# Kernel tuning notes

Measured on AMD Instinct MI355X. Metric: run time of the kernel, lower is better.

Reference implementation:

```python
import jax, jax.numpy as jnp
import numpy as np

B, T, F, H = 8, 1024, 1024, 16
DK = F // H


def setup_inputs() -> dict:
    key = jax.random.key(0)
    ks = jax.random.split(key, 12)
    s = 1.0 / np.sqrt(F)
    return {
        "query": jax.random.normal(ks[0], (B, T, F), jnp.float32),
        "key": jax.random.normal(ks[1], (B, T, F), jnp.float32),
        "value": jax.random.normal(ks[2], (B, T, F), jnp.float32),
        "mask": jnp.ones((B, T), jnp.float32),
        "Wq": jax.random.normal(ks[3], (F, F), jnp.float32) * s,
        "bq": jax.random.normal(ks[4], (F,), jnp.float32) * s,
        "Wk": jax.random.normal(ks[5], (F, F), jnp.float32) * s,
        "bk": jax.random.normal(ks[6], (F,), jnp.float32) * s,
        "Wv": jax.random.normal(ks[7], (F, F), jnp.float32) * s,
        "bv": jax.random.normal(ks[8], (F,), jnp.float32) * s,
        "Wo": jax.random.normal(ks[9], (F, F), jnp.float32) * s,
        "bo": jax.random.normal(ks[10], (F,), jnp.float32) * s,
    }


def reference(query, key, value, mask, Wq, bq, Wk, bk, Wv, bv, Wo, bo):
    # projections, split into heads: (B, H, T, DK)
    def proj(x, W, b):
        y = x @ W.T + b
        return y.reshape(B, -1, H, DK).transpose(0, 2, 1, 3)

    q = proj(query, Wq, bq)
    k = proj(key, Wk, bk)
    v = proj(value, Wv, bv)

    scores = jnp.einsum("bhqd,bhkd->bhqk", q, k) / jnp.sqrt(jnp.float32(DK))
    attn = jax.nn.softmax(scores, axis=-1)  # dropout is identity (eval / p=0)
    x = jnp.einsum("bhqk,bhkd->bhqd", attn, v)
    x = x.transpose(0, 2, 1, 3).reshape(B, -1, F)
    x = x @ Wo.T + bo
    return x * mask[..., None]
```

## Files before the change

### kernel.cpp

```cpp
#include <hip/hip_runtime.h>
#include <hip/hip_bf16.h>

typedef unsigned short u16;
typedef unsigned int u32;
typedef __attribute__((ext_vector_type(8))) short bf16x8;
typedef __attribute__((ext_vector_type(8))) unsigned short u16x8;
typedef __attribute__((ext_vector_type(4))) unsigned short u16x4;
typedef __attribute__((ext_vector_type(4))) float f32x4;

#define DEVI __device__ __forceinline__

static constexpr int Bn = 8, Tn = 1024, Fn = 1024, Hn = 16, DKn = 64;
static constexpr int Mtot = Bn * Tn;

DEVI u16 f2bf(float x) {
  unsigned u = __builtin_bit_cast(unsigned, x);
  u += 0x7fffu + ((u >> 16) & 1u);
  return (u16)(u >> 16);
}

DEVI u32 cvt_pk_bf16(float lo, float hi) {
  u32 r;
  asm("v_cvt_pk_bf16_f32 %0, %1, %2" : "=v"(r) : "v"(lo), "v"(hi));
  return r;
}

DEVI f32x4 mfma16(bf16x8 a, bf16x8 b, f32x4 c) {
  return __builtin_amdgcn_mfma_f32_16x16x32_bf16(a, b, c, 0, 0, 0);
}

typedef const __attribute__((address_space(1))) void GAS;
typedef __attribute__((address_space(3))) void LAS;
#define GLL16(gp, lp) __builtin_amdgcn_global_load_lds((GAS*)(gp), (LAS*)(lp), 16, 0, 0)

DEVI void cvt_chunk(const float* __restrict__ in, u16* __restrict__ out, int i) {
  const float4* p = reinterpret_cast<const float4*>(in + i);
  float4 a = p[0], b = p[1];
  float v[8] = {a.x, a.y, a.z, a.w, b.x, b.y, b.z, b.w};
  u16x8 r;
#pragma unroll
  for (int j = 0; j < 8; j++) r[j] = f2bf(v[j]);
  *reinterpret_cast<u16x8*>(out + i) = r;
}

__global__ __launch_bounds__(256) void cvt3(const float* __restrict__ a, const float* __restrict__ b,
                                            const float* __restrict__ c, u16* __restrict__ oa,
                                            u16* __restrict__ ob, u16* __restrict__ oc) {
  const int id = blockIdx.x * 256 + threadIdx.x;
  const int seg = id >> 20;
  const int off = (id & 1048575) * 8;
  const float* s = seg == 0 ? a : (seg == 1 ? b : c);
  u16* d = seg == 0 ? oa : (seg == 1 ? ob : oc);
  cvt_chunk(s, d, off);
}

__global__ __launch_bounds__(256) void cvt4(const float* __restrict__ a, const float* __restrict__ b,
                                            const float* __restrict__ c, const float* __restrict__ e,
                                            u16* __restrict__ oa, u16* __restrict__ ob,
                                            u16* __restrict__ oc, u16* __restrict__ oe) {
  const int id = blockIdx.x * 256 + threadIdx.x;
  const int seg = id >> 17;
  const int off = (id & 131071) * 8;
  const float* s = seg == 0 ? a : (seg == 1 ? b : (seg == 2 ? c : e));
  u16* d = seg == 0 ? oa : (seg == 1 ? ob : (seg == 2 ? oc : oe));
  cvt_chunk(s, d, off);
}

template <int MODE>
__global__ __launch_bounds__(512, 1) void gemm8(const u16* __restrict__ A,
                                                const u16* __restrict__ Bw,
                                                const float* __restrict__ bias,
                                                const float* __restrict__ mask,
                                                u16* __restrict__ Obf,
                                                float* __restrict__ Of,
                                                float oscale) {
  constexpr int Kd = 1024;
  __shared__ u16 sA[2][256 * 64];
  __shared__ u16 sB[2][128 * 64];
  const int tid = threadIdx.x;
  const int l = tid & 63, w = tid >> 6;
  const int wm = w >> 1, wn = w & 1;
  const int lr = l & 15, g = l >> 4;
  const int bid = blockIdx.x;
  const int wg = (bid & 7) * 32 + (bid >> 3);
  const int m0 = (wg >> 3) * 256, n0 = (wg & 7) * 128;

  f32x4 acc[4][4];
#pragma unroll
  for (int i = 0; i < 4; i++)
#pragma unroll
    for (int j = 0; j < 4; j++) acc[i][j] = f32x4{0.f, 0.f, 0.f, 0.f};

  int aoff[4], boff[2];
#pragma unroll
  for (int i = 0; i < 4; i++) {
    const int c = i * 512 + tid;
    const int r = c >> 3, cc = (c & 7) ^ (r & 7);
    aoff[i] = r * Kd + cc * 8;
  }
#pragma unroll
  for (int i = 0; i < 2; i++) {
    const int c = i * 512 + tid;
    const int r = c >> 3, cc = (c & 7) ^ (r & 7);
    boff[i] = r * Kd + cc * 8;
  }
  const u16* Abase = A + (size_t)m0 * Kd;
  const u16* Bbase = Bw + (size_t)n0 * Kd;

  auto stage = [&](int buf, int kt) {
#pragma unroll
    for (int i = 0; i < 4; i++)
      GLL16(Abase + kt * 64 + aoff[i], (char*)&sA[buf][0] + (i * 512 + w * 64) * 16);
#pragma unroll
    for (int i = 0; i < 2; i++)
      GLL16(Bbase + kt * 64 + boff[i], (char*)&sB[buf][0] + (i * 512 + w * 64) * 16);
  };

  stage(0, 0);
  for (int t = 0; t < 16; ++t) {
    const int cur = t & 1;
    if (t < 15) {
      stage(cur ^ 1, t + 1);
      asm volatile("s_waitcnt vmcnt(6)" ::: "memory");
    } else {
      asm volatile("s_waitcnt vmcnt(0)" ::: "memory");
    }
    asm volatile("s_barrier" ::: "memory");
#pragma unroll
    for (int ks = 0; ks < 2; ks++) {
      bf16x8 af[4], bfr[4];
#pragma unroll
      for (int mi = 0; mi < 4; mi++) {
        const int row = wm * 64 + mi * 16 + lr;
        af[mi] = *reinterpret_cast<const bf16x8*>(
            (const char*)&sA[cur][0] + row * 128 + ((ks * 64 + g * 16) ^ ((row & 7) << 4)));
      }
#pragma unroll
      for (int ni = 0; ni < 4; ni++) {
        const int row = wn * 64 + ni * 16 + lr;
        bfr[ni] = *reinterpret_cast<const bf16x8*>(
            (const char*)&sB[cur][0] + row * 128 + ((ks * 64 + g * 16) ^ ((row & 7) << 4)));
      }
      __builtin_amdgcn_s_setprio(1);
#pragma unroll
      for (int mi = 0; mi < 4; mi++)
#pragma unroll
        for (int ni = 0; ni < 4; ni++) {
          if constexpr (MODE == 1)
            acc[mi][ni] = mfma16(af[mi], bfr[ni], acc[mi][ni]);
          else
            acc[ni][mi] = mfma16(bfr[ni], af[mi], acc[ni][mi]);
        }
      __builtin_amdgcn_s_setprio(0);
    }
    asm volatile("s_barrier" ::: "memory");
  }

  if constexpr (MODE == 1) {
#pragma unroll
    for (int ni = 0; ni < 4; ni++) {
      const int n = n0 + wn * 64 + ni * 16 + lr;
      const float bv = bias[n];
      const int h = n >> 6, dk = n & 63;
#pragma unroll
      for (int mi = 0; mi < 4; mi++) {
        const int mb = m0 + wm * 64 + mi * 16 + g * 4;
        u16x4 pk;
#pragma unroll
        for (int j = 0; j < 4; j++) pk[j] = f2bf(acc[mi][ni][j] + bv);
        const int b = mb >> 10, tt = mb & 1023;
        size_t idx = (((size_t)b * 16 + h) * 64 + dk) * 1024 + tt;
        *reinterpret_cast<u16x4*>(Obf + idx) = pk;
      }
    }
  } else {
#pragma unroll
    for (int ni = 0; ni < 4; ni++) {
      const int nb = n0 + wn * 64 + ni * 16 + g * 4;
      const float4 b4 = *reinterpret_cast<const float4*>(&bias[nb]);
#pragma unroll
      for (int mi = 0; mi < 4; mi++) {
        const int m = m0 + wm * 64 + mi * 16 + lr;
        const f32x4 a = acc[ni][mi];
        if constexpr (MODE == 0) {
          const int b = m >> 10, tt = m & 1023;
          const int h = nb >> 6, dk0 = nb & 63;
          u16x4 pk;
          pk[0] = f2bf((a[0] + b4.x) * oscale);
          pk[1] = f2bf((a[1] + b4.y) * oscale);
          pk[2] = f2bf((a[2] + b4.z) * oscale);
          pk[3] = f2bf((a[3] + b4.w) * oscale);
          *reinterpret_cast<u16x4*>(&Obf[((((size_t)b * 16 + h) * 1024 + tt) * 64) + dk0]) = pk;
        } else {
          const float mk = mask[m];
          float4 o;
          o.x = (a[0] + b4.x) * mk;
          o.y = (a[1] + b4.y) * mk;
          o.z = (a[2] + b4.z) * mk;
          o.w = (a[3] + b4.w) * mk;
          *reinterpret_cast<float4*>(&Of[(size_t)m * 1024 + nb]) = o;
        }
      }
    }
  }
}

__global__ __launch_bounds__(256, 4) void flash_attn(const u16* __restrict__ Qb,
                                                     const u16* __restrict__ Kb,
                                                     const u16* __restrict__ Vt,
                                                     u16* __restrict__ ctx) {
  __shared__ u16 sK[2][64 * 64];
  __shared__ u16 sV[64 * 64];
  __shared__ u16 pbuf[4][16 * 64];
  const int tid = threadIdx.x, l = tid & 63, w = tid >> 6;
  const int lr = l & 15, g = l >> 4;
  const int wg = ((blockIdx.x & 7) << 7) + (blockIdx.x >> 3);
  const int qt = wg & 7, bh = wg >> 3;
  const u16* Qh = Qb + (size_t)bh * (Tn * DKn);
  const u16* Kh = Kb + (size_t)bh * (Tn * DKn);
  const u16* Vh = Vt + (size_t)bh * (Tn * DKn);

  bf16x8 aq[2][2];
  int qrow[2];
#pragma unroll
  for (int qg = 0; qg < 2; qg++) {
    qrow[qg] = qt * 128 + w * 32 + qg * 16 + lr;
    aq[qg][0] = *reinterpret_cast<const bf16x8*>(Qh + (size_t)qrow[qg] * 64 + g * 8);
    aq[qg][1] = *reinterpret_cast<const bf16x8*>(Qh + (size_t)qrow[qg] * 64 + 32 + g * 8);
  }

  float mrow[2] = {-1e30f, -1e30f}, lsum[2] = {0.f, 0.f};
  f32x4 of[2][4];
#pragma unroll
  for (int qg = 0; qg < 2; qg++)
#pragma unroll
    for (int c = 0; c < 4; c++) of[qg][c] = f32x4{0.f, 0.f, 0.f, 0.f};

  char* pb = (char*)&pbuf[w][0];
  const int sw = (lr & 7) << 4;
  int wadr[4];
#pragma unroll
  for (int c = 0; c < 4; c++) wadr[c] = lr * 128 + (((c * 16 + g * 4) * 2) ^ sw);
  const int radr0 = lr * 128 + ((g * 16) ^ sw);
  const int radr1 = lr * 128 + ((64 + g * 16) ^ sw);

  auto stageK = [&](int buf, int kv0) {
#pragma unroll
    for (int i = 0; i < 2; i++) {
      const int tt = i * 256 + tid;
      const int r = tt >> 3;
      const int c = (tt & 7) ^ (r & 7);
      GLL16((const char*)Kh + ((size_t)(kv0 + r) << 7) + (c << 4),
            (char*)&sK[buf][0] + i * 4096 + w * 1024);
    }
  };
  auto stageV = [&](int kv0) {
#pragma unroll
    for (int i = 0; i < 2; i++) {
      const int tt = i * 256 + tid;
      const int r = tt >> 3;
      const int c = (tt & 7) ^ (r & 7);
      GLL16((const char*)Vh + ((size_t)r << 11) + kv0 * 2 + (c << 4),
            (char*)&sV[0] + i * 4096 + w * 1024);
    }
  };

  stageK(0, 0);
  stageV(0);
  __syncthreads();
  int cur = 0;

  for (int t = 0; t < 16; t++) {
    if (t < 15) stageK(cur ^ 1, (t + 1) * 64);
    const char* kb = (const char*)&sK[cur][0];
    const char* vb = (const char*)&sV[0];

    f32x4 sf[2][4];
    __builtin_amdgcn_s_setprio(1);
#pragma unroll
    for (int c = 0; c < 4; c++) {
      const char* kr = kb + (c * 16 + lr) * 128;
      bf16x8 k0 = *reinterpret_cast<const bf16x8*>(kr + ((g * 16) ^ sw));
      bf16x8 k1 = *reinterpret_cast<const bf16x8*>(kr + ((64 + g * 16) ^ sw));
      f32x4 z0 = mfma16(k0, aq[0][0], f32x4{0.f, 0.f, 0.f, 0.f});
      sf[0][c] = mfma16(k1, aq[0][1], z0);
      f32x4 z1 = mfma16(k0, aq[1][0], f32x4{0.f, 0.f, 0.f, 0.f});
      sf[1][c] = mfma16(k1, aq[1][1], z1);
    }
    __builtin_amdgcn_s_setprio(0);

    bf16x8 ap[2][2];
#pragma unroll
    for (int qg = 0; qg < 2; qg++) {
      f32x4 mx4 = sf[qg][0];
#pragma unroll
      for (int c = 1; c < 4; c++)
#pragma unroll
        for (int j = 0; j < 4; j++) mx4[j] = fmaxf(mx4[j], sf[qg][c][j]);
      const float pmax = fmaxf(fmaxf(mx4[0], mx4[1]), fmaxf(mx4[2], mx4[3]));
      if (__any(pmax > mrow[qg] + 8.0f)) {
        float mx = pmax;
        mx = fmaxf(mx, __shfl_xor(mx, 16));
        mx = fmaxf(mx, __shfl_xor(mx, 32));
        const float mn = fmaxf(mrow[qg], mx);
        const float alpha = exp2f(mrow[qg] - mn);
        mrow[qg] = mn;
        lsum[qg] *= alpha;
#pragma unroll
        for (int c = 0; c < 4; c++)
#pragma unroll
          for (int j = 0; j < 4; j++) of[qg][c][j] *= alpha;
      }
      const float mn = mrow[qg];
      float rs = 0.f;
#pragma unroll
      for (int c = 0; c < 4; c++)
#pragma unroll
        for (int j = 0; j < 4; j++) {
          float p = exp2f(sf[qg][c][j] - mn);
          sf[qg][c][j] = p;
          rs += p;
        }
      lsum[qg] += rs;

#pragma unroll
      for (int c = 0; c < 4; c++) {
        uint2 pk;
        pk.x = cvt_pk_bf16(sf[qg][c][0], sf[qg][c][1]);
        pk.y = cvt_pk_bf16(sf[qg][c][2], sf[qg][c][3]);
        *reinterpret_cast<uint2*>(pb + wadr[c]) = pk;
      }
      ap[qg][0] = *reinterpret_cast<const bf16x8*>(pb + radr0);
      ap[qg][1] = *reinterpret_cast<const bf16x8*>(pb + radr1);
    }

    __syncthreads();

    __builtin_amdgcn_s_setprio(1);
#pragma unroll
    for (int d0 = 0; d0 < 4; d0++) {
      const char* vr = vb + (d0 * 16 + lr) * 128;
      bf16x8 v0 = *reinterpret_cast<const bf16x8*>(vr + ((g * 16) ^ sw));
      bf16x8 v1 = *reinterpret_cast<const bf16x8*>(vr + ((64 + g * 16) ^ sw));
#pragma unroll
      for (int qg = 0; qg < 2; qg++) {
        f32x4 z = mfma16(v0, ap[qg][0], of[qg][d0]);
        of[qg][d0] = mfma16(v1, ap[qg][1], z);
      }
    }
    __builtin_amdgcn_s_setprio(0);

    __syncthreads();
    if (t < 15) stageV((t + 1) * 64);
    cur ^= 1;
  }

  const int b = bh >> 4, h = bh & 15;
#pragma unroll
  for (int qg = 0; qg < 2; qg++) {
    float ls = lsum[qg];
    ls += __shfl_xor(ls, 16);
    ls += __shfl_xor(ls, 32);
    const float inv = 1.0f / ls;
    const size_t base = ((size_t)b * 1024 + qrow[qg]) * 1024 + h * 64;
#pragma unroll
    for (int d0 = 0; d0 < 4; d0++) {
      uint2 pk;
      pk.x = cvt_pk_bf16(of[qg][d0][0] * inv, of[qg][d0][1] * inv);
      pk.y = cvt_pk_bf16(of[qg][d0][2] * inv, of[qg][d0][3] * inv);
      *reinterpret_cast<uint2*>(ctx + base + d0 * 16 + g * 4) = pk;
    }
  }
}

extern "C" void kernel_launch(void* const* d_in, const int* in_sizes, int n_in,
                              void* d_out, int out_size, void* d_ws, size_t ws_size,
                              hipStream_t stream) {
  const float* query = (const float*)d_in[0];
  const float* key = (const float*)d_in[1];
  const float* value = (const float*)d_in[2];
  const float* mask = (const float*)d_in[3];
  const float* Wq = (const float*)d_in[4];
  const float* bq = (const float*)d_in[5];
  const float* Wk = (const float*)d_in[6];
  const float* bk = (const float*)d_in[7];
  const float* Wv = (const float*)d_in[8];
  const float* bv = (const float*)d_in[9];
  const float* Wo = (const float*)d_in[10];
  const float* bo = (const float*)d_in[11];
  (void)in_sizes; (void)n_in; (void)out_size; (void)ws_size;

  u16* ws = (u16*)d_ws;
  const size_t MB8 = (size_t)8 << 20;
  u16* Xq = ws;
  u16* Xk = ws + MB8;
  u16* Xv = ws + 2 * MB8;
  u16* Wqb = ws + 3 * MB8;
  u16* Wkb = Wqb + (1 << 20);
  u16* Wvb = Wkb + (1 << 20);
  u16* Wob = Wvb + (1 << 20);
  u16* Qb = Wob + (1 << 20);
  u16* Kb = Qb + MB8;
  u16* Vtb = Kb + MB8;
  u16* ctx = Xq;

  cvt3<<<12288, 256, 0, stream>>>(query, key, value, Xq, Xk, Xv);
  cvt4<<<2048, 256, 0, stream>>>(Wq, Wk, Wv, Wo, Wqb, Wkb, Wvb, Wob);

  const float SC = 0.125f * 1.44269504089f;
  const int ng = (Mtot / 256) * (Fn / 128);
  gemm8<0><<<ng, 512, 0, stream>>>(Xq, Wqb, bq, nullptr, Qb, nullptr, SC);
  gemm8<0><<<ng, 512, 0, stream>>>(Xk, Wkb, bk, nullptr, Kb, nullptr, 1.0f);
  gemm8<1><<<ng, 512, 0, stream>>>(Xv, Wvb, bv, nullptr, Vtb, nullptr, 1.0f);

  flash_attn<<<Bn * Hn * (Tn / 128), 256, 0, stream>>>(Qb, Kb, Vtb, ctx);

  gemm8<2><<<ng, 512, 0, stream>>>(ctx, Wob, bo, mask, nullptr, (float*)d_out, 1.0f);
}
```

Before: 198.1 us.

## Halve flash-attention query tile to 64 rows per block

Each attention workgroup now covers 64 query rows, one 16-row MFMA group per wave, instead of 128 rows with two groups per wave. The grid doubles to 2048 blocks and launch bounds rise to 5 blocks per CU, with the block-to-(batch, head, tile) mapping updated to match. The aim is to cut register pressure and raise occupancy and latency hiding. In exchange, every K/V tile staged in LDS is reused by half as many queries, doubling K/V staging traffic per unit of work. The output-projection GEMM launch count is written as a literal equal to the previous computed value.

```diff
diff --git a/kernel.cpp b/kernel.cpp
--- a/kernel.cpp
+++ b/kernel.cpp
@@ -205,7 +205,7 @@
   }
 }
 
-__global__ __launch_bounds__(256, 4) void flash_attn(const u16* __restrict__ Qb,
+__global__ __launch_bounds__(256, 5) void flash_attn(const u16* __restrict__ Qb,
                                                      const u16* __restrict__ Kb,
                                                      const u16* __restrict__ Vt,
                                                      u16* __restrict__ ctx) {
@@ -214,27 +214,20 @@
   __shared__ u16 pbuf[4][16 * 64];
   const int tid = threadIdx.x, l = tid & 63, w = tid >> 6;
   const int lr = l & 15, g = l >> 4;
-  const int wg = ((blockIdx.x & 7) << 7) + (blockIdx.x >> 3);
-  const int qt = wg & 7, bh = wg >> 3;
+  const int wg = ((blockIdx.x & 7) << 8) + (blockIdx.x >> 3);
+  const int qt = wg & 15, bh = wg >> 4;
   const u16* Qh = Qb + (size_t)bh * (Tn * DKn);
   const u16* Kh = Kb + (size_t)bh * (Tn * DKn);
   const u16* Vh = Vt + (size_t)bh * (Tn * DKn);
 
-  bf16x8 aq[2][2];
-  int qrow[2];
-#pragma unroll
-  for (int qg = 0; qg < 2; qg++) {
-    qrow[qg] = qt * 128 + w * 32 + qg * 16 + lr;
-    aq[qg][0] = *reinterpret_cast<const bf16x8*>(Qh + (size_t)qrow[qg] * 64 + g * 8);
-    aq[qg][1] = *reinterpret_cast<const bf16x8*>(Qh + (size_t)qrow[qg] * 64 + 32 + g * 8);
-  }
-
-  float mrow[2] = {-1e30f, -1e30f}, lsum[2] = {0.f, 0.f};
-  f32x4 of[2][4];
-#pragma unroll
-  for (int qg = 0; qg < 2; qg++)
-#pragma unroll
-    for (int c = 0; c < 4; c++) of[qg][c] = f32x4{0.f, 0.f, 0.f, 0.f};
+  const int qrow = qt * 64 + w * 16 + lr;
+  const bf16x8 aq0 = *reinterpret_cast<const bf16x8*>(Qh + (size_t)qrow * 64 + g * 8);
+  const bf16x8 aq1 = *reinterpret_cast<const bf16x8*>(Qh + (size_t)qrow * 64 + 32 + g * 8);
+
+  float mrow = -1e30f, lsum = 0.f;
+  f32x4 of[4];
+#pragma unroll
+  for (int c = 0; c < 4; c++) of[c] = f32x4{0.f, 0.f, 0.f, 0.f};
 
   char* pb = (char*)&pbuf[w][0];
   const int sw = (lr & 7) << 4;
@@ -275,64 +268,57 @@
     const char* kb = (const char*)&sK[cur][0];
     const char* vb = (const char*)&sV[0];
 
-    f32x4 sf[2][4];
+    f32x4 sf[4];
     __builtin_amdgcn_s_setprio(1);
 #pragma unroll
     for (int c = 0; c < 4; c++) {
       const char* kr = kb + (c * 16 + lr) * 128;
       bf16x8 k0 = *reinterpret_cast<const bf16x8*>(kr + ((g * 16) ^ sw));
       bf16x8 k1 = *reinterpret_cast<const bf16x8*>(kr + ((64 + g * 16) ^ sw));
-      f32x4 z0 = mfma16(k0, aq[0][0], f32x4{0.f, 0.f, 0.f, 0.f});
-      sf[0][c] = mfma16(k1, aq[0][1], z0);
-      f32x4 z1 = mfma16(k0, aq[1][0], f32x4{0.f, 0.f, 0.f, 0.f});
-      sf[1][c] = mfma16(k1, aq[1][1], z1);
+      f32x4 z = mfma16(k0, aq0, f32x4{0.f, 0.f, 0.f, 0.f});
+      sf[c] = mfma16(k1, aq1, z);
     }
     __builtin_amdgcn_s_setprio(0);
 
-    bf16x8 ap[2][2];
-#pragma unroll
-    for (int qg = 0; qg < 2; qg++) {
-      f32x4 mx4 = sf[qg][0];
-#pragma unroll
-      for (int c = 1; c < 4; c++)
-#pragma unroll
-        for (int j = 0; j < 4; j++) mx4[j] = fmaxf(mx4[j], sf[qg][c][j]);
-      const float pmax = fmaxf(fmaxf(mx4[0], mx4[1]), fmaxf(mx4[2], mx4[3]));
-      if (__any(pmax > mrow[qg] + 8.0f)) {
-        float mx = pmax;
-        mx = fmaxf(mx, __shfl_xor(mx, 16));
-        mx = fmaxf(mx, __shfl_xor(mx, 32));
-        const float mn = fmaxf(mrow[qg], mx);
-        const float alpha = exp2f(mrow[qg] - mn);
-        mrow[qg] = mn;
-        lsum[qg] *= alpha;
-#pragma unroll
-        for (int c = 0; c < 4; c++)
-#pragma unroll
-          for (int j = 0; j < 4; j++) of[qg][c][j] *= alpha;
-      }
-      const float mn = mrow[qg];
-      float rs = 0.f;
+    f32x4 mx4 = sf[0];
+#pragma unroll
+    for (int c = 1; c < 4; c++)
+#pragma unroll
+      for (int j = 0; j < 4; j++) mx4[j] = fmaxf(mx4[j], sf[c][j]);
+    const float pmax = fmaxf(fmaxf(mx4[0], mx4[1]), fmaxf(mx4[2], mx4[3]));
+    if (__any(pmax > mrow + 8.0f)) {
+      float mx = pmax;
+      mx = fmaxf(mx, __shfl_xor(mx, 16));
+      mx = fmaxf(mx, __shfl_xor(mx, 32));
+      const float mn = fmaxf(mrow, mx);
+      const float alpha = exp2f(mrow - mn);
+      mrow = mn;
+      lsum *= alpha;
 #pragma unroll
       for (int c = 0; c < 4; c++)
 #pragma unroll
-        for (int j = 0; j < 4; j++) {
-          float p = exp2f(sf[qg][c][j] - mn);
-          sf[qg][c][j] = p;
-          rs += p;
-        }
-      lsum[qg] += rs;
-
-#pragma unroll
-      for (int c = 0; c < 4; c++) {
-        uint2 pk;
-        pk.x = cvt_pk_bf16(sf[qg][c][0], sf[qg][c][1]);
-        pk.y = cvt_pk_bf16(sf[qg][c][2], sf[qg][c][3]);
-        *reinterpret_cast<uint2*>(pb + wadr[c]) = pk;
-      }
-      ap[qg][0] = *reinterpret_cast<const bf16x8*>(pb + radr0);
-      ap[qg][1] = *reinterpret_cast<const bf16x8*>(pb + radr1);
-    }
+        for (int j = 0; j < 4; j++) of[c][j] *= alpha;
+    }
+    float rs = 0.f;
+#pragma unroll
+    for (int c = 0; c < 4; c++)
+#pragma unroll
+      for (int j = 0; j < 4; j++) {
+        float pp = exp2f(sf[c][j] - mrow);
+        sf[c][j] = pp;
+        rs += pp;
+      }
+    lsum += rs;
+
+#pragma unroll
+    for (int c = 0; c < 4; c++) {
+      uint2 pk;
+      pk.x = cvt_pk_bf16(sf[c][0], sf[c][1]);
+      pk.y = cvt_pk_bf16(sf[c][2], sf[c][3]);
+      *reinterpret_cast<uint2*>(pb + wadr[c]) = pk;
+    }
+    const bf16x8 ap0 = *reinterpret_cast<const bf16x8*>(pb + radr0);
+    const bf16x8 ap1 = *reinterpret_cast<const bf16x8*>(pb + radr1);
 
     __syncthreads();
 
@@ -342,11 +328,8 @@
       const char* vr = vb + (d0 * 16 + lr) * 128;
       bf16x8 v0 = *reinterpret_cast<const bf16x8*>(vr + ((g * 16) ^ sw));
       bf16x8 v1 = *reinterpret_cast<const bf16x8*>(vr + ((64 + g * 16) ^ sw));
-#pragma unroll
-      for (int qg = 0; qg < 2; qg++) {
-        f32x4 z = mfma16(v0, ap[qg][0], of[qg][d0]);
-        of[qg][d0] = mfma16(v1, ap[qg][1], z);
-      }
+      f32x4 z = mfma16(v0, ap0, of[d0]);
+      of[d0] = mfma16(v1, ap1, z);
     }
     __builtin_amdgcn_s_setprio(0);
 
@@ -355,21 +338,18 @@
     cur ^= 1;
   }
 
+  float ls = lsum;
+  ls += __shfl_xor(ls, 16);
+  ls += __shfl_xor(ls, 32);
+  const float inv = 1.0f / ls;
   const int b = bh >> 4, h = bh & 15;
-#pragma unroll
-  for (int qg = 0; qg < 2; qg++) {
-    float ls = lsum[qg];
-    ls += __shfl_xor(ls, 16);
-    ls += __shfl_xor(ls, 32);
-    const float inv = 1.0f / ls;
-    const size_t base = ((size_t)b * 1024 + qrow[qg]) * 1024 + h * 64;
-#pragma unroll
-    for (int d0 = 0; d0 < 4; d0++) {
-      uint2 pk;
-      pk.x = cvt_pk_bf16(of[qg][d0][0] * inv, of[qg][d0][1] * inv);
-      pk.y = cvt_pk_bf16(of[qg][d0][2] * inv, of[qg][d0][3] * inv);
-      *reinterpret_cast<uint2*>(ctx + base + d0 * 16 + g * 4) = pk;
-    }
+  const size_t base = ((size_t)b * 1024 + qrow) * 1024 + h * 64;
+#pragma unroll
+  for (int d0 = 0; d0 < 4; d0++) {
+    uint2 pk;
+    pk.x = cvt_pk_bf16(of[d0][0] * inv, of[d0][1] * inv);
+    pk.y = cvt_pk_bf16(of[d0][2] * inv, of[d0][3] * inv);
+    *reinterpret_cast<uint2*>(ctx + base + d0 * 16 + g * 4) = pk;
   }
 }
 
@@ -413,7 +393,7 @@
   gemm8<0><<<ng, 512, 0, stream>>>(Xk, Wkb, bk, nullptr, Kb, nullptr, 1.0f);
   gemm8<1><<<ng, 512, 0, stream>>>(Xv, Wvb, bv, nullptr, Vtb, nullptr, 1.0f);
 
-  flash_attn<<<Bn * Hn * (Tn / 128), 256, 0, stream>>>(Qb, Kb, Vtb, ctx);
-
-  gemm8<2><<<ng, 512, 0, stream>>>(ctx, Wob, bo, mask, nullptr, (float*)d_out, 1.0f);
-}
+  flash_attn<<<Bn * Hn * (Tn / 64), 256, 0, stream>>>(Qb, Kb, Vtb, ctx);
+
+  gemm8<2><<<256, 512, 0, stream>>>(ctx, Wob, bo, mask, nullptr, (float*)d_out, 1.0f);
+}
```

Result: slower. 204.1 us (+3.1%).

## Merge Q/K/V projection GEMMs into one launch and split A/B staging

Applied to the files above, without the earlier changes.

The three separate projection GEMM launches become a single launch with a 3-wide grid dimension that selects inputs, weights, bias and output layout per block. This removes two kernel launches and the tail idle time at the end of each one. The GEMM core now prefetches the A tile before the barrier but issues the B tile prefetch after the first k-substep's MFMAs, which spreads global loads across compute. In exchange, the runtime branch on the projection index adds code size and register pressure, and the different wait count changes how much load latency the pipeline hides.

```diff
diff --git a/kernel.cpp b/kernel.cpp
--- a/kernel.cpp
+++ b/kernel.cpp
@@ -66,15 +66,171 @@
   cvt_chunk(s, d, off);
 }
 
-template <int MODE>
-__global__ __launch_bounds__(512, 1) void gemm8(const u16* __restrict__ A,
-                                                const u16* __restrict__ Bw,
-                                                const float* __restrict__ bias,
-                                                const float* __restrict__ mask,
-                                                u16* __restrict__ Obf,
-                                                float* __restrict__ Of,
-                                                float oscale) {
+template <int SWAP>
+DEVI void gemm_core_run(const u16* __restrict__ A, const u16* __restrict__ Bw,
+                        int m0, int n0, int tid, u16* sA0, u16* sA1, u16* sB0, u16* sB1,
+                        f32x4 (&acc)[4][4]) {
   constexpr int Kd = 1024;
+  const int l = tid & 63, w = tid >> 6;
+  const int wm = w >> 1, wn = w & 1;
+  const int lr = l & 15, g = l >> 4;
+
+  int aoff[4], boff[2];
+#pragma unroll
+  for (int i = 0; i < 4; i++) {
+    const int c = i * 512 + tid;
+    const int r = c >> 3, cc = (c & 7) ^ (r & 7);
+    aoff[i] = r * Kd + cc * 8;
+  }
+#pragma unroll
+  for (int i = 0; i < 2; i++) {
+    const int c = i * 512 + tid;
+    const int r = c >> 3, cc = (c & 7) ^ (r & 7);
+    boff[i] = r * Kd + cc * 8;
+  }
+  const u16* Ab = A + (size_t)m0 * Kd;
+  const u16* Bb = Bw + (size_t)n0 * Kd;
+  u16* sAp[2] = {sA0, sA1};
+  u16* sBp[2] = {sB0, sB1};
+
+  auto stageA = [&](int buf, int kt) {
+#pragma unroll
+    for (int i = 0; i < 4; i++)
+      GLL16(Ab + kt * 64 + aoff[i], (char*)sAp[buf] + (i * 512 + w * 64) * 16);
+  };
+  auto stageB = [&](int buf, int kt) {
+#pragma unroll
+    for (int i = 0; i < 2; i++)
+      GLL16(Bb + kt * 64 + boff[i], (char*)sBp[buf] + (i * 512 + w * 64) * 16);
+  };
+
+  stageA(0, 0);
+  stageB(0, 0);
+  for (int t = 0; t < 16; ++t) {
+    const int cur = t & 1;
+    const char* cA = (const char*)sAp[cur];
+    const char* cB = (const char*)sBp[cur];
+    if (t < 15) {
+      stageA(cur ^ 1, t + 1);
+      asm volatile("s_waitcnt vmcnt(4)" ::: "memory");
+    } else {
+      asm volatile("s_waitcnt vmcnt(0)" ::: "memory");
+    }
+    asm volatile("s_barrier" ::: "memory");
+#pragma unroll
+    for (int ks = 0; ks < 2; ks++) {
+      bf16x8 af[4], bfr[4];
+#pragma unroll
+      for (int mi = 0; mi < 4; mi++) {
+        const int row = wm * 64 + mi * 16 + lr;
+        af[mi] = *reinterpret_cast<const bf16x8*>(cA + row * 128 +
+                                                  ((ks * 64 + g * 16) ^ ((row & 7) << 4)));
+      }
+#pragma unroll
+      for (int ni = 0; ni < 4; ni++) {
+        const int row = wn * 64 + ni * 16 + lr;
+        bfr[ni] = *reinterpret_cast<const bf16x8*>(cB + row * 128 +
+                                                   ((ks * 64 + g * 16) ^ ((row & 7) << 4)));
+      }
+      __builtin_amdgcn_s_setprio(1);
+#pragma unroll
+      for (int mi = 0; mi < 4; mi++)
+#pragma unroll
+        for (int ni = 0; ni < 4; ni++) {
+          if constexpr (SWAP)
+            acc[ni][mi] = mfma16(bfr[ni], af[mi], acc[ni][mi]);
+          else
+            acc[mi][ni] = mfma16(af[mi], bfr[ni], acc[mi][ni]);
+        }
+      __builtin_amdgcn_s_setprio(0);
+      if (ks == 0 && t < 15) stageB(cur ^ 1, t + 1);
+    }
+    asm volatile("s_barrier" ::: "memory");
+  }
+}
+
+DEVI void gemm_core_run_rt(const u16* __restrict__ A, const u16* __restrict__ Bw,
+                           int m0, int n0, int tid, bool swap, u16* sA0, u16* sA1,
+                           u16* sB0, u16* sB1, f32x4 (&acc)[4][4]) {
+  if (swap)
+    gemm_core_run<1>(A, Bw, m0, n0, tid, sA0, sA1, sB0, sB1, acc);
+  else
+    gemm_core_run<0>(A, Bw, m0, n0, tid, sA0, sA1, sB0, sB1, acc);
+}
+
+__global__ __launch_bounds__(512, 1) void qkv_gemm(
+    const u16* __restrict__ Xq, const u16* __restrict__ Xk, const u16* __restrict__ Xv,
+    const u16* __restrict__ Wq, const u16* __restrict__ Wk, const u16* __restrict__ Wv,
+    const float* __restrict__ bq, const float* __restrict__ bk, const float* __restrict__ bv,
+    u16* __restrict__ Qo, u16* __restrict__ Ko, u16* __restrict__ Vo, float SC) {
+  __shared__ u16 sA[2][256 * 64];
+  __shared__ u16 sB[2][128 * 64];
+  const int tid = threadIdx.x;
+  const int l = tid & 63, w = tid >> 6;
+  const int wm = w >> 1, wn = w & 1;
+  const int lr = l & 15, g = l >> 4;
+  const int p = blockIdx.y;
+  const u16* A = p == 0 ? Xq : (p == 1 ? Xk : Xv);
+  const u16* Bw = p == 0 ? Wq : (p == 1 ? Wk : Wv);
+  const float* bias = p == 0 ? bq : (p == 1 ? bk : bv);
+  u16* Obf = p == 0 ? Qo : (p == 1 ? Ko : Vo);
+  const float oscale = p == 0 ? SC : 1.0f;
+  const int bid = blockIdx.x;
+  const int wg = (bid & 7) * 32 + (bid >> 3);
+  const int m0 = (wg >> 3) * 256, n0 = (wg & 7) * 128;
+
+  f32x4 acc[4][4];
+#pragma unroll
+  for (int i = 0; i < 4; i++)
+#pragma unroll
+    for (int j = 0; j < 4; j++) acc[i][j] = f32x4{0.f, 0.f, 0.f, 0.f};
+
+  gemm_core_run_rt(A, Bw, m0, n0, tid, p != 2, sA[0], sA[1], sB[0], sB[1], acc);
+
+  if (p == 2) {
+#pragma unroll
+    for (int ni = 0; ni < 4; ni++) {
+      const int n = n0 + wn * 64 + ni * 16 + lr;
+      const float bvv = bias[n];
+      const int h = n >> 6, dk = n & 63;
+#pragma unroll
+      for (int mi = 0; mi < 4; mi++) {
+        const int mb = m0 + wm * 64 + mi * 16 + g * 4;
+        u16x4 pk;
+#pragma unroll
+        for (int j = 0; j < 4; j++) pk[j] = f2bf(acc[mi][ni][j] + bvv);
+        const int b = mb >> 10, tt = mb & 1023;
+        size_t idx = (((size_t)b * 16 + h) * 64 + dk) * 1024 + tt;
+        *reinterpret_cast<u16x4*>(Obf + idx) = pk;
+      }
+    }
+  } else {
+#pragma unroll
+    for (int ni = 0; ni < 4; ni++) {
+      const int nb = n0 + wn * 64 + ni * 16 + g * 4;
+      const float4 b4 = *reinterpret_cast<const float4*>(&bias[nb]);
+#pragma unroll
+      for (int mi = 0; mi < 4; mi++) {
+        const int m = m0 + wm * 64 + mi * 16 + lr;
+        const f32x4 a = acc[ni][mi];
+        const int b = m >> 10, tt = m & 1023;
+        const int h = nb >> 6, dk0 = nb & 63;
+        u16x4 pk;
+        pk[0] = f2bf((a[0] + b4.x) * oscale);
+        pk[1] = f2bf((a[1] + b4.y) * oscale);
+        pk[2] = f2bf((a[2] + b4.z) * oscale);
+        pk[3] = f2bf((a[3] + b4.w) * oscale);
+        *reinterpret_cast<u16x4*>(&Obf[((((size_t)b * 16 + h) * 1024 + tt) * 64) + dk0]) = pk;
+      }
+    }
+  }
+}
+
+__global__ __launch_bounds__(512, 1) void gemm_out(const u16* __restrict__ A,
+                                                   const u16* __restrict__ Bw,
+                                                   const float* __restrict__ bias,
+                                                   const float* __restrict__ mask,
+                                                   float* __restrict__ Of) {
   __shared__ u16 sA[2][256 * 64];
   __shared__ u16 sB[2][128 * 64];
   const int tid = threadIdx.x;
@@ -91,116 +247,23 @@
 #pragma unroll
     for (int j = 0; j < 4; j++) acc[i][j] = f32x4{0.f, 0.f, 0.f, 0.f};
 
-  int aoff[4], boff[2];
-#pragma unroll
-  for (int i = 0; i < 4; i++) {
-    const int c = i * 512 + tid;
-    const int r = c >> 3, cc = (c & 7) ^ (r & 7);
-    aoff[i] = r * Kd + cc * 8;
-  }
-#pragma unroll
-  for (int i = 0; i < 2; i++) {
-    const int c = i * 512 + tid;
-    const int r = c >> 3, cc = (c & 7) ^ (r & 7);
-    boff[i] = r * Kd + cc * 8;
-  }
-  const u16* Abase = A + (size_t)m0 * Kd;
-  const u16* Bbase = Bw + (size_t)n0 * Kd;
-
-  auto stage = [&](int buf, int kt) {
-#pragma unroll
-    for (int i = 0; i < 4; i++)
-      GLL16(Abase + kt * 64 + aoff[i], (char*)&sA[buf][0] + (i * 512 + w * 64) * 16);
-#pragma unroll
-    for (int i = 0; i < 2; i++)
-      GLL16(Bbase + kt * 64 + boff[i], (char*)&sB[buf][0] + (i * 512 + w * 64) * 16);
-  };
-
-  stage(0, 0);
-  for (int t = 0; t < 16; ++t) {
-    const int cur = t & 1;
-    if (t < 15) {
-      stage(cur ^ 1, t + 1);
-      asm volatile("s_waitcnt vmcnt(6)" ::: "memory");
-    } else {
-      asm volatile("s_waitcnt vmcnt(0)" ::: "memory");
-    }
-    asm volatile("s_barrier" ::: "memory");
-#pragma unroll
-    for (int ks = 0; ks < 2; ks++) {
-      bf16x8 af[4], bfr[4];
-#pragma unroll
-      for (int mi = 0; mi < 4; mi++) {
-        const int row = wm * 64 + mi * 16 + lr;
-        af[mi] = *reinterpret_cast<const bf16x8*>(
-            (const char*)&sA[cur][0] + row * 128 + ((ks * 64 + g * 16) ^ ((row & 7) << 4)));
-      }
-#pragma unroll
-      for (int ni = 0; ni < 4; ni++) {
-        const int row = wn * 64 + ni * 16 + lr;
-        bfr[ni] = *reinterpret_cast<const bf16x8*>(
-            (const char*)&sB[cur][0] + row * 128 + ((ks * 64 + g * 16) ^ ((row & 7) << 4)));
-      }
-      __builtin_amdgcn_s_setprio(1);
-#pragma unroll
-      for (int mi = 0; mi < 4; mi++)
-#pragma unroll
-        for (int ni = 0; ni < 4; ni++) {
-          if constexpr (MODE == 1)
-            acc[mi][ni] = mfma16(af[mi], bfr[ni], acc[mi][ni]);
-          else
-            acc[ni][mi] = mfma16(bfr[ni], af[mi], acc[ni][mi]);
-        }
-      __builtin_amdgcn_s_setprio(0);
-    }
-    asm volatile("s_barrier" ::: "memory");
-  }
-
-  if constexpr (MODE == 1) {
-#pragma unroll
-    for (int ni = 0; ni < 4; ni++) {
-      const int n = n0 + wn * 64 + ni * 16 + lr;
-      const float bv = bias[n];
-      const int h = n >> 6, dk = n & 63;
-#pragma unroll
-      for (int mi = 0; mi < 4; mi++) {
-        const int mb = m0 + wm * 64 + mi * 16 + g * 4;
-        u16x4 pk;
-#pragma unroll
-        for (int j = 0; j < 4; j++) pk[j] = f2bf(acc[mi][ni][j] + bv);
-        const int b = mb >> 10, tt = mb & 1023;
-        size_t idx = (((size_t)b * 16 + h) * 64 + dk) * 1024 + tt;
-        *reinterpret_cast<u16x4*>(Obf + idx) = pk;
-      }
-    }
-  } else {
-#pragma unroll
-    for (int ni = 0; ni < 4; ni++) {
-      const int nb = n0 + wn * 64 + ni * 16 + g * 4;
-      const float4 b4 = *reinterpret_cast<const float4*>(&bias[nb]);
-#pragma unroll
-      for (int mi = 0; mi < 4; mi++) {
-        const int m = m0 + wm * 64 + mi * 16 + lr;
-        const f32x4 a = acc[ni][mi];
-        if constexpr (MODE == 0) {
-          const int b = m >> 10, tt = m & 1023;
-          const int h = nb >> 6, dk0 = nb & 63;
-          u16x4 pk;
-          pk[0] = f2bf((a[0] + b4.x) * oscale);
-          pk[1] = f2bf((a[1] + b4.y) * oscale);
-          pk[2] = f2bf((a[2] + b4.z) * oscale);
-          pk[3] = f2bf((a[3] + b4.w) * oscale);
-          *reinterpret_cast<u16x4*>(&Obf[((((size_t)b * 16 + h) * 1024 + tt) * 64) + dk0]) = pk;
-        } else {
-          const float mk = mask[m];
-          float4 o;
-          o.x = (a[0] + b4.x) * mk;
-          o.y = (a[1] + b4.y) * mk;
-          o.z = (a[2] + b4.z) * mk;
-          o.w = (a[3] + b4.w) * mk;
-          *reinterpret_cast<float4*>(&Of[(size_t)m * 1024 + nb]) = o;
-        }
-      }
+  gemm_core_run<1>(A, Bw, m0, n0, tid, sA[0], sA[1], sB[0], sB[1], acc);
+
+#pragma unroll
+  for (int ni = 0; ni < 4; ni++) {
+    const int nb = n0 + wn * 64 + ni * 16 + g * 4;
+    const float4 b4 = *reinterpret_cast<const float4*>(&bias[nb]);
+#pragma unroll
+    for (int mi = 0; mi < 4; mi++) {
+      const int m = m0 + wm * 64 + mi * 16 + lr;
+      const f32x4 a = acc[ni][mi];
+      const float mk = mask[m];
+      float4 o;
+      o.x = (a[0] + b4.x) * mk;
+      o.y = (a[1] + b4.y) * mk;
+      o.z = (a[2] + b4.z) * mk;
+      o.w = (a[3] + b4.w) * mk;
+      *reinterpret_cast<float4*>(&Of[(size_t)m * 1024 + nb]) = o;
     }
   }
 }
@@ -317,9 +380,9 @@
       for (int c = 0; c < 4; c++)
 #pragma unroll
         for (int j = 0; j < 4; j++) {
-          float p = exp2f(sf[qg][c][j] - mn);
-          sf[qg][c][j] = p;
-          rs += p;
+          float pp = exp2f(sf[qg][c][j] - mn);
+          sf[qg][c][j] = pp;
+          rs += pp;
         }
       lsum[qg] += rs;
 
@@ -408,12 +471,10 @@
   cvt4<<<2048, 256, 0, stream>>>(Wq, Wk, Wv, Wo, Wqb, Wkb, Wvb, Wob);
 
   const float SC = 0.125f * 1.44269504089f;
-  const int ng = (Mtot / 256) * (Fn / 128);
-  gemm8<0><<<ng, 512, 0, stream>>>(Xq, Wqb, bq, nullptr, Qb, nullptr, SC);
-  gemm8<0><<<ng, 512, 0, stream>>>(Xk, Wkb, bk, nullptr, Kb, nullptr, 1.0f);
-  gemm8<1><<<ng, 512, 0, stream>>>(Xv, Wvb, bv, nullptr, Vtb, nullptr, 1.0f);
+  qkv_gemm<<<dim3(256, 3), 512, 0, stream>>>(Xq, Xk, Xv, Wqb, Wkb, Wvb, bq, bk, bv,
+                                             Qb, Kb, Vtb, SC);
 
   flash_attn<<<Bn * Hn * (Tn / 128), 256, 0, stream>>>(Qb, Kb, Vtb, ctx);
 
-  gemm8<2><<<ng, 512, 0, stream>>>(ctx, Wob, bo, mask, nullptr, (float*)d_out, 1.0f);
-}
+  gemm_out<<<256, 512, 0, stream>>>(ctx, Wob, bo, mask, (float*)d_out);
+}
```

Result: slower. 232.0 us (+17.1%).
